# Kernel optimization log

Measured on AMD Instinct MI355X. Metric: run time of the kernel, lower is better.

## Reference

```python
import math
import jax, jax.numpy as jnp
import numpy as np

B, S, DK, DV = 8, 2048, 512, 512

def setup_inputs() -> dict:
    key = jax.random.key(0)
    kq, kk, kv, km = jax.random.split(key, 4)
    Q = jax.random.normal(kq, (B, S, DK), dtype=jnp.float32)
    K = jax.random.normal(kk, (B, S, DK), dtype=jnp.float32)
    V = jax.random.normal(kv, (B, S, DV), dtype=jnp.float32)
    # key-padding mask, True = masked out; broadcasts over query dim
    mask_out = jax.random.randint(km, (B, 1, S), 0, 2).astype(jnp.bool_)
    return {"Q": Q, "K": K, "V": V, "mask_out": mask_out}

def reference(Q, K, V, mask_out):
    scale = math.sqrt(Q.shape[-1])
    # [B, S, S] scores
    scores = jnp.einsum('bqd,bkd->bqk', Q, K) / scale
    scores = jnp.where(mask_out, -jnp.inf, scores)
    attn = jax.nn.softmax(scores, axis=-1)
    # dropout is identity in eval mode (reference baseline)
    return jnp.einsum('bqk,bkv->bqv', attn, V)
```

## Files before the change

kernel.cpp:

```cpp
#include <hip/hip_runtime.h>
#include <stdint.h>
#include <stddef.h>

#define B_ 8
#define S_ 2048
#define D_ 512
#define QT 64
#define KTL 32
#define NIT (S_ / KTL)

typedef __attribute__((ext_vector_type(8))) short short8;
typedef __attribute__((ext_vector_type(4))) float f32x4;

#define OFF_K0  0
#define OFF_K1  32768
#define OFF_ST  65536
#define OFF_P   73728
#define OFF_A   77824
#define OFF_HM  78080
#define OFF_L   78592
#define OFF_M   79104
#define LDS_BYTES 79360

__device__ __forceinline__ void gl_lds16(const void* g, void* l) {
  __builtin_amdgcn_global_load_lds(
      (const __attribute__((address_space(1))) uint32_t*)g,
      (__attribute__((address_space(3))) uint32_t*)l, 16, 0, 0);
}

__device__ __forceinline__ void bar_lgkm() {
  __asm__ __volatile__("" ::: "memory");
  __builtin_amdgcn_s_waitcnt(0xC07F);
  __builtin_amdgcn_s_barrier();
  __asm__ __volatile__("" ::: "memory");
}
__device__ __forceinline__ void bar_vm0() {
  __asm__ __volatile__("" ::: "memory");
  __builtin_amdgcn_s_waitcnt(0x0070);
  __builtin_amdgcn_s_barrier();
  __asm__ __volatile__("" ::: "memory");
}

template<int CTRL>
__device__ __forceinline__ float dpp_mov(float x) {
  return __builtin_bit_cast(float,
      __builtin_amdgcn_update_dpp(0, __builtin_bit_cast(int, x),
                                  CTRL, 0xF, 0xF, true));
}
__device__ __forceinline__ float red8_max(float x) {
  x = fmaxf(x, dpp_mov<0xB1>(x));
  x = fmaxf(x, dpp_mov<0x4E>(x));
  x = fmaxf(x, dpp_mov<0x141>(x));
  return x;
}
__device__ __forceinline__ float red8_sum(float x) {
  x += dpp_mov<0xB1>(x);
  x += dpp_mov<0x4E>(x);
  x += dpp_mov<0x141>(x);
  return x;
}

__device__ __forceinline__ uint32_t f2bf(float f) {
  union { float f; uint32_t u; } x; x.f = f;
  uint32_t r = x.u + 0x7FFFu + ((x.u >> 16) & 1u);
  return r >> 16;
}

__device__ __forceinline__ bool sniff_fp32(const void* p) {
  const uint32_t* w = (const uint32_t*)p;
  bool ok = true;
  #pragma unroll 1
  for (int i = 0; i < 64; ++i) {
    uint32_t e = (w[i] >> 23) & 0xFFu;
    if (!(e == 0u || (e >= 64u && e <= 192u))) ok = false;
  }
  return ok;
}

__device__ __forceinline__ short8 cvt8(const void* src, bool fp32) {
  short8 d;
  if (fp32) {
    const float* s = (const float*)src;
    f32x4 a = *(const f32x4*)s, c = *(const f32x4*)(s + 4);
    #pragma unroll
    for (int j = 0; j < 4; ++j) { d[j] = (short)f2bf(a[j]); d[4 + j] = (short)f2bf(c[j]); }
  } else {
    d = *(const short8*)src;
  }
  return d;
}

__global__ void prep_kernel(const void* __restrict__ K, const void* __restrict__ V,
                            uint16_t* __restrict__ kbf, uint16_t* __restrict__ vt) {
  __shared__ uint32_t vtile[64 * 32];
  bool fp32 = sniff_fp32(K);
  int kt = blockIdx.x, dt = blockIdx.y, b = blockIdx.z;
  int t  = threadIdx.x;
  {
    size_t off = (size_t)b * S_ * D_ + (size_t)(kt * 64 + (t >> 3)) * D_ + dt * 64 + (t & 7) * 8;
    const void* src = fp32 ? (const void*)((const float*)K + off)
                           : (const void*)((const uint16_t*)K + off);
    *(short8*)(kbf + off) = cvt8(src, fp32);
  }
  {
    int key = t >> 3;
    int c0  = (t & 7) * 4;
    size_t off = (size_t)b * S_ * D_ + (size_t)(kt * 64 + key) * D_ + dt * 64 + (t & 7) * 8;
    const void* src = fp32 ? (const void*)((const float*)V + off)
                           : (const void*)((const uint16_t*)V + off);
    short8 d = cvt8(src, fp32);
    const uint32_t* dw = (const uint32_t*)&d;
    #pragma unroll
    for (int i = 0; i < 4; ++i)
      vtile[key * 32 + ((c0 + i + key) & 31)] = dw[i];
  }
  __syncthreads();
  {
    int dvl = t >> 3;
    int kg  = t & 7;
    short8 o;
    #pragma unroll
    for (int j = 0; j < 8; ++j) {
      int key = kg * 8 + j;
      uint32_t wv = vtile[key * 32 + (((dvl >> 1) + key) & 31)];
      o[j] = (short)((dvl & 1) ? (wv >> 16) : (wv & 0xFFFFu));
    }
    *(short8*)(vt + ((size_t)b * D_ + dt * 64 + dvl) * S_ + kt * 64 + kg * 8) = o;
  }
}

__device__ __forceinline__ void stage_K(char* buf, const uint16_t* kg, int w, int lane, int kt) {
  #pragma unroll
  for (int p = 0; p < 4; ++p) {
    int n = p * 8 + w;
    int g = (lane & ~7) | ((lane ^ n) & 7);
    gl_lds16(kg + ((size_t)(kt * KTL + n)) * D_ + g * 8, buf + n * 1024);
  }
}
__device__ __forceinline__ void stage_K_slow(char* buf, const void* kg, bool fp32,
                                             int w, int lane, int kt) {
  #pragma unroll
  for (int p = 0; p < 4; ++p) {
    int n = p * 8 + w;
    size_t off = ((size_t)(kt * KTL + n)) * D_ + lane * 8;
    const void* src = fp32 ? (const void*)((const float*)kg + off)
                           : (const void*)((const uint16_t*)kg + off);
    short8 d = cvt8(src, fp32);
    int s = (lane & ~7) | ((lane ^ n) & 7);
    *(short8*)(buf + n * 1024 + s * 16) = d;
  }
}
__device__ __forceinline__ void stage_V_slow(char* smem, const void* vg, bool fp32,
                                             int w, int lane, int kt) {
  #pragma unroll
  for (int p = 0; p < 4; ++p) {
    int n = p * 8 + w;
    size_t off = ((size_t)(kt * KTL + n)) * D_ + lane * 8;
    const void* src = fp32 ? (const void*)((const float*)vg + off)
                           : (const void*)((const uint16_t*)vg + off);
    short8 d = cvt8(src, fp32);
    *(short8*)(smem + OFF_K1 + n * 1024 + lane * 16) = d;
  }
}

template<bool FAST>
__global__ __launch_bounds__(512, 2)
void attn_kernel(const void* __restrict__ Q, const void* __restrict__ K,
                 const void* __restrict__ V, const void* __restrict__ mask,
                 const uint16_t* __restrict__ kbf, const uint16_t* __restrict__ vtbf,
                 void* __restrict__ out) {
  extern __shared__ char smem[];
  const int tid  = threadIdx.x;
  const int lane = tid & 63;
  const int w    = tid >> 6;
  const int m15  = lane & 15;
  const int kq   = lane >> 4;

  const bool fp32 = sniff_fp32(Q);

  const int b     = blockIdx.x;
  const int qbase = blockIdx.y * QT;
  const int qt_w  = w >> 1;
  const int kh    = w & 1;

  const uint16_t* kgf  = FAST ? (kbf + (size_t)b * S_ * D_) : nullptr;
  const uint16_t* vtg  = FAST ? (vtbf + (size_t)b * D_ * S_) : nullptr;
  const void* kgs = fp32 ? (const void*)((const float*)K + (size_t)b * S_ * D_)
                         : (const void*)((const uint16_t*)K + (size_t)b * S_ * D_);
  const void* vgs = fp32 ? (const void*)((const float*)V + (size_t)b * S_ * D_)
                         : (const void*)((const uint16_t*)V + (size_t)b * S_ * D_);

  if (tid < 64) {
    const uint32_t* mw = (const uint32_t*)mask;
    const uint8_t*  mb = (const uint8_t*)mask;
    bool is64 = true, any_even = false, is32 = true;
    for (int j = 0; j < 64; ++j) {
      uint32_t lo = mw[2 * j], hi = mw[2 * j + 1];
      if (hi != 0u || lo > 1u) is64 = false;
      if (lo) any_even = true;
    }
    is64 = is64 && any_even;
    for (int j = 0; j < 128; ++j) {
      uint32_t x = mw[j];
      if (x != 0u && x != 1u && x != 0x3F800000u) is32 = false;
    }
    uint32_t bits = 0;
    int base = b * S_ + tid * 32;
    for (int e = 0; e < 32; ++e) {
      uint32_t x = is64 ? mw[2 * (base + e)]
                        : (is32 ? mw[base + e] : (uint32_t)mb[base + e]);
      bits |= (x ? 1u : 0u) << e;
    }
    *(uint32_t*)(smem + OFF_M + tid * 4) = bits;
  }

  short8 aq[16];
  {
    size_t q0 = ((size_t)b * S_ + qbase + qt_w * 16 + m15) * D_ + kq * 8;
    #pragma unroll
    for (int sl = 0; sl < 16; ++sl) {
      size_t off = q0 + sl * 32;
      const void* src = fp32 ? (const void*)((const float*)Q + off)
                             : (const void*)((const uint16_t*)Q + off);
      aq[sl] = cvt8(src, fp32);
    }
  }

  f32x4 acc_o[4][4];
  #pragma unroll
  for (int i = 0; i < 4; ++i)
    #pragma unroll
    for (int j = 0; j < 4; ++j)
      acc_o[i][j] = (f32x4){0.f, 0.f, 0.f, 0.f};

  float m_run = -1e30f, l_run = 0.f;
  const float k1 = 0.06375872f;

  const int nql = kh * 16 + m15;
  const int qsw = qt_w * 16 + m15;

  if constexpr (FAST) {
    stage_K(smem + OFF_K0, kgf, w, lane, 0);

    #pragma unroll 1
    for (int kt = 0; kt < NIT; ++kt) {
      char* kbuf = smem + ((kt & 1) ? OFF_K1 : OFF_K0);
      bar_vm0();

      short8 vf[4];
      #pragma unroll
      for (int ct = 0; ct < 4; ++ct)
        vf[ct] = *(const short8*)(vtg + (size_t)(w * 64 + ct * 16 + m15) * S_
                                  + kt * KTL + kq * 8);
      if (kt < NIT - 1)
        stage_K(smem + ((kt & 1) ? OFF_K0 : OFF_K1), kgf, w, lane, kt + 1);

      f32x4 acc_s0 = (f32x4){0.f, 0.f, 0.f, 0.f};
      f32x4 acc_s1 = (f32x4){0.f, 0.f, 0.f, 0.f};
      #pragma unroll
      for (int sl = 0; sl < 8; ++sl) {
        int c0  = sl * 4 + kq;
        int c1  = (sl + 8) * 4 + kq;
        int cs0 = (c0 & ~7) | ((c0 ^ nql) & 7);
        int cs1 = (c1 & ~7) | ((c1 ^ nql) & 7);
        short8 b0 = *(const short8*)(kbuf + nql * 1024 + cs0 * 16);
        short8 b1 = *(const short8*)(kbuf + nql * 1024 + cs1 * 16);
        acc_s0 = __builtin_amdgcn_mfma_f32_16x16x32_bf16(b0, aq[sl],     acc_s0, 0, 0, 0);
        acc_s1 = __builtin_amdgcn_mfma_f32_16x16x32_bf16(b1, aq[sl + 8], acc_s1, 0, 0, 0);
      }

      uint32_t mword = *(const uint32_t*)(smem + OFF_M + kt * 4);
      float u[4];
      #pragma unroll
      for (int r = 0; r < 4; ++r) {
        float bv = ((mword >> (kh * 16 + kq * 4 + r)) & 1u) ? -3.0e38f : 0.f;
        u[r] = (acc_s0[r] + acc_s1[r]) * k1 + bv;
      }
      float hm = fmaxf(fmaxf(u[0], u[1]), fmaxf(u[2], u[3]));
      hm = fmaxf(hm, __shfl_xor(hm, 16, 64));
      hm = fmaxf(hm, __shfl_xor(hm, 32, 64));
      if (lane < 16)
        *(float*)(smem + OFF_HM + qsw * 8 + kh * 4) = hm;
      bar_lgkm();

      float other = *(const float*)(smem + OFF_HM + qsw * 8 + (1 - kh) * 4);
      float m_new = fmaxf(m_run, fmaxf(hm, other));
      float alpha = exp2f(m_run - m_new);
      m_run = m_new;
      float s = 0.f;
      #pragma unroll
      for (int r = 0; r < 4; ++r) { u[r] = exp2f(u[r] - m_new); s += u[r]; }
      s += __shfl_xor(s, 16, 64);
      s += __shfl_xor(s, 32, 64);
      l_run = l_run * alpha + s;
      uint2 d;
      d.x = f2bf(u[0]) | (f2bf(u[1]) << 16);
      d.y = f2bf(u[2]) | (f2bf(u[3]) << 16);
      int g0 = kh * 2 + (kq >> 1);
      int g  = g0 ^ (qsw & 3);
      *(uint2*)(smem + OFF_P + qsw * 64 + g * 16 + (kq & 1) * 8) = d;
      if (kh == 0 && lane < 16)
        *(float*)(smem + OFF_A + qsw * 4) = alpha;
      bar_lgkm();

      #pragma unroll
      for (int rt = 0; rt < 4; ++rt) {
        f32x4 al = *(const f32x4*)(smem + OFF_A + (rt * 16 + kq * 4) * 4);
        #pragma unroll
        for (int ct = 0; ct < 4; ++ct) acc_o[rt][ct] *= al;
      }
      short8 ap[4];
      #pragma unroll
      for (int rt = 0; rt < 4; ++rt) {
        int rr = rt * 16 + m15;
        int gg = kq ^ (rr & 3);
        ap[rt] = *(const short8*)(smem + OFF_P + rr * 64 + gg * 16);
      }
      #pragma unroll
      for (int ct = 0; ct < 4; ++ct)
        #pragma unroll
        for (int rt = 0; rt < 4; ++rt)
          acc_o[rt][ct] = __builtin_amdgcn_mfma_f32_16x16x32_bf16(
              ap[rt], vf[ct], acc_o[rt][ct], 0, 0, 0);
    }

    if (lane < 16)
      *(float*)(smem + OFF_L + qsw * 8 + kh * 4) = l_run;
    __syncthreads();

    #pragma unroll
    for (int rt = 0; rt < 4; ++rt) {
      #pragma unroll
      for (int ct = 0; ct < 4; ++ct) {
        int col = w * 64 + ct * 16 + m15;
        #pragma unroll
        for (int r = 0; r < 4; ++r) {
          int row = rt * 16 + kq * 4 + r;
          float lt = *(const float*)(smem + OFF_L + row * 8)
                   + *(const float*)(smem + OFF_L + row * 8 + 4);
          float inv = lt > 0.f ? 1.f / lt : 0.f;
          size_t idx = ((size_t)b * S_ + qbase + row) * D_ + col;
          float val = acc_o[rt][ct][r] * inv;
          if (fp32) ((float*)out)[idx] = val;
          else      ((uint16_t*)out)[idx] = (uint16_t)f2bf(val);
        }
      }
    }
  } else {
    #pragma unroll 1
    for (int kt = 0; kt < NIT; ++kt) {
      __syncthreads();
      stage_K_slow(smem + OFF_K0, kgs, fp32, w, lane, kt);
      stage_V_slow(smem, vgs, fp32, w, lane, kt);
      __syncthreads();

      int keyg = kt * KTL + nql;
      float bv = ((*(const uint32_t*)(smem + OFF_M + (keyg >> 5) * 4) >> (keyg & 31)) & 1u)
                 ? -3.0e38f : 0.f;
      f32x4 a0 = {0.f,0.f,0.f,0.f}, a1 = {0.f,0.f,0.f,0.f};
      #pragma unroll
      for (int sl = 0; sl < 8; ++sl) {
        int c0  = sl * 4 + kq;
        int c1  = (sl + 8) * 4 + kq;
        int cs0 = (c0 & ~7) | ((c0 ^ nql) & 7);
        int cs1 = (c1 & ~7) | ((c1 ^ nql) & 7);
        short8 bf0 = *(const short8*)(smem + OFF_K0 + nql * 1024 + cs0 * 16);
        short8 bf1 = *(const short8*)(smem + OFF_K0 + nql * 1024 + cs1 * 16);
        a0 = __builtin_amdgcn_mfma_f32_16x16x32_bf16(aq[sl],     bf0, a0, 0, 0, 0);
        a1 = __builtin_amdgcn_mfma_f32_16x16x32_bf16(aq[sl + 8], bf1, a1, 0, 0, 0);
      }
      {
        int blk  = qt_w * 4 + kq;
        int xblk = blk ^ (nql & 15) ^ ((nql >> 2) & 3);
        f32x4 sv;
        #pragma unroll
        for (int r = 0; r < 4; ++r) sv[r] = (a0[r] + a1[r]) * k1 + bv;
        *(f32x4*)(smem + OFF_ST + nql * 256 + xblk * 16) = sv;
      }
      bar_lgkm();

      {
        int r  = w * 8 + (lane >> 3);
        int k0 = (lane & 7) * 4;
        float u[4];
        #pragma unroll
        for (int i = 0; i < 4; ++i) {
          int k    = k0 + i;
          int xblk = (r >> 2) ^ (k & 15) ^ ((k >> 2) & 3);
          u[i] = *(const float*)(smem + OFF_ST + k * 256 + xblk * 16 + (r & 3) * 4);
        }
        float mt = fmaxf(fmaxf(u[0], u[1]), fmaxf(u[2], u[3]));
        mt = red8_max(mt);
        float m_new = fmaxf(m_run, mt);
        float alpha = exp2f(m_run - m_new);
        float s = 0.f;
        #pragma unroll
        for (int i = 0; i < 4; ++i) { u[i] = exp2f(u[i] - m_new); s += u[i]; }
        s = red8_sum(s);
        l_run = l_run * alpha + s;
        m_run = m_new;
        uint2 d;
        d.x = f2bf(u[0]) | (f2bf(u[1]) << 16);
        d.y = f2bf(u[2]) | (f2bf(u[3]) << 16);
        int g = ((lane & 7) >> 1) ^ (r & 3);
        *(uint2*)(smem + OFF_P + r * 64 + g * 16 + (lane & 1) * 8) = d;
        if ((lane & 7) == 0) {
          *(float*)(smem + OFF_A + r * 4) = alpha;
          *(float*)(smem + OFF_L + r * 4) = l_run;
        }
      }
      bar_lgkm();

      #pragma unroll
      for (int rt = 0; rt < 4; ++rt) {
        f32x4 al = *(const f32x4*)(smem + OFF_A + (rt * 16 + kq * 4) * 4);
        #pragma unroll
        for (int ct = 0; ct < 4; ++ct) acc_o[rt][ct] *= al;
      }
      short8 ap[4];
      #pragma unroll
      for (int rt = 0; rt < 4; ++rt) {
        int rr = rt * 16 + m15;
        int g  = kq ^ (rr & 3);
        ap[rt] = *(const short8*)(smem + OFF_P + rr * 64 + g * 16);
      }
      #pragma unroll
      for (int ct = 0; ct < 4; ++ct) {
        short8 bvv;
        #pragma unroll
        for (int j = 0; j < 8; ++j)
          bvv[j] = *(const short*)(smem + OFF_K1 + (kq * 8 + j) * 1024
                                   + (w * 64 + ct * 16 + m15) * 2);
        #pragma unroll
        for (int rt = 0; rt < 4; ++rt)
          acc_o[rt][ct] = __builtin_amdgcn_mfma_f32_16x16x32_bf16(
              ap[rt], bvv, acc_o[rt][ct], 0, 0, 0);
      }
    }

    #pragma unroll
    for (int rt = 0; rt < 4; ++rt) {
      f32x4 lv = *(const f32x4*)(smem + OFF_L + (rt * 16 + kq * 4) * 4);
      f32x4 inv;
      #pragma unroll
      for (int r = 0; r < 4; ++r) inv[r] = lv[r] > 0.f ? 1.f / lv[r] : 0.f;
      #pragma unroll
      for (int ct = 0; ct < 4; ++ct) {
        int col = w * 64 + ct * 16 + m15;
        #pragma unroll
        for (int r = 0; r < 4; ++r) {
          int row = qbase + rt * 16 + kq * 4 + r;
          size_t idx = ((size_t)b * S_ + row) * D_ + col;
          float val = acc_o[rt][ct][r] * inv[r];
          if (fp32) ((float*)out)[idx] = val;
          else      ((uint16_t*)out)[idx] = (uint16_t)f2bf(val);
        }
      }
    }
  }
}

extern "C" void kernel_launch(void* const* d_in, const int* in_sizes, int n_in,
                              void* d_out, int out_size, void* d_ws, size_t ws_size,
                              hipStream_t stream) {
  (void)in_sizes; (void)n_in; (void)out_size;
  const void* Q    = d_in[0];
  const void* K    = d_in[1];
  const void* V    = d_in[2];
  const void* mask = d_in[3];

  const size_t half = (size_t)B_ * S_ * D_ * 2;
  bool fast = ws_size >= 2 * half;

  if (fast) {
    uint16_t* kbf  = (uint16_t*)d_ws;
    uint16_t* vtbf = (uint16_t*)((char*)d_ws + half);
    prep_kernel<<<dim3(32, 8, 8), 512, 0, stream>>>(K, V, kbf, vtbf);
    hipFuncSetAttribute((const void*)attn_kernel<true>,
                        hipFuncAttributeMaxDynamicSharedMemorySize, LDS_BYTES);
    attn_kernel<true><<<dim3(8, S_ / QT), 512, LDS_BYTES, stream>>>(
        Q, K, V, mask, kbf, vtbf, d_out);
  } else {
    hipFuncSetAttribute((const void*)attn_kernel<false>,
                        hipFuncAttributeMaxDynamicSharedMemorySize, LDS_BYTES);
    attn_kernel<false><<<dim3(8, S_ / QT), 512, LDS_BYTES, stream>>>(
        Q, K, V, mask, nullptr, nullptr, d_out);
  }
}
```

Measured before the change: 306.9 us.

## Double key tile to 64 and restructure softmax through staged LDS scores

Raises the per-iteration key tile from 32 to 64 in the fast path, halving the number of barrier-separated iterations. Each wave now computes scores for 32 queries by 16 keys, sharing each K fragment across two MFMAs, and writes them to LDS. A row-wise softmax pass then reads them back with 8-lane reductions instead of cross-wave half-max exchange. LDS use roughly doubles to about 153 KB, which together with 32 Q fragments per thread likely prevents two blocks per CU and adds register pressure.

```diff
diff --git a/kernel.cpp b/kernel.cpp
--- a/kernel.cpp
+++ b/kernel.cpp
@@ -6,21 +6,22 @@
 #define S_ 2048
 #define D_ 512
 #define QT 64
-#define KTL 32
+#define KTL 64
 #define NIT (S_ / KTL)
+#define KTLS 32
+#define NITS (S_ / KTLS)
 
 typedef __attribute__((ext_vector_type(8))) short short8;
 typedef __attribute__((ext_vector_type(4))) float f32x4;
 
 #define OFF_K0  0
-#define OFF_K1  32768
-#define OFF_ST  65536
-#define OFF_P   73728
-#define OFF_A   77824
-#define OFF_HM  78080
-#define OFF_L   78592
-#define OFF_M   79104
-#define LDS_BYTES 79360
+#define OFF_K1  65536
+#define OFF_ST  131072
+#define OFF_P   147456
+#define OFF_A   155648
+#define OFF_L   155904
+#define OFF_M   156160
+#define LDS_BYTES 156416
 
 __device__ __forceinline__ void gl_lds16(const void* g, void* l) {
   __builtin_amdgcn_global_load_lds(
@@ -131,7 +132,7 @@
 
 __device__ __forceinline__ void stage_K(char* buf, const uint16_t* kg, int w, int lane, int kt) {
   #pragma unroll
-  for (int p = 0; p < 4; ++p) {
+  for (int p = 0; p < 8; ++p) {
     int n = p * 8 + w;
     int g = (lane & ~7) | ((lane ^ n) & 7);
     gl_lds16(kg + ((size_t)(kt * KTL + n)) * D_ + g * 8, buf + n * 1024);
@@ -142,7 +143,7 @@
   #pragma unroll
   for (int p = 0; p < 4; ++p) {
     int n = p * 8 + w;
-    size_t off = ((size_t)(kt * KTL + n)) * D_ + lane * 8;
+    size_t off = ((size_t)(kt * KTLS + n)) * D_ + lane * 8;
     const void* src = fp32 ? (const void*)((const float*)kg + off)
                            : (const void*)((const uint16_t*)kg + off);
     short8 d = cvt8(src, fp32);
@@ -155,7 +156,7 @@
   #pragma unroll
   for (int p = 0; p < 4; ++p) {
     int n = p * 8 + w;
-    size_t off = ((size_t)(kt * KTL + n)) * D_ + lane * 8;
+    size_t off = ((size_t)(kt * KTLS + n)) * D_ + lane * 8;
     const void* src = fp32 ? (const void*)((const float*)vg + off)
                            : (const void*)((const uint16_t*)vg + off);
     short8 d = cvt8(src, fp32);
@@ -180,8 +181,6 @@
 
   const int b     = blockIdx.x;
   const int qbase = blockIdx.y * QT;
-  const int qt_w  = w >> 1;
-  const int kh    = w & 1;
 
   const uint16_t* kgf  = FAST ? (kbf + (size_t)b * S_ * D_) : nullptr;
   const uint16_t* vtg  = FAST ? (vtbf + (size_t)b * D_ * S_) : nullptr;
@@ -214,18 +213,6 @@
     *(uint32_t*)(smem + OFF_M + tid * 4) = bits;
   }
 
-  short8 aq[16];
-  {
-    size_t q0 = ((size_t)b * S_ + qbase + qt_w * 16 + m15) * D_ + kq * 8;
-    #pragma unroll
-    for (int sl = 0; sl < 16; ++sl) {
-      size_t off = q0 + sl * 32;
-      const void* src = fp32 ? (const void*)((const float*)Q + off)
-                             : (const void*)((const uint16_t*)Q + off);
-      aq[sl] = cvt8(src, fp32);
-    }
-  }
-
   f32x4 acc_o[4][4];
   #pragma unroll
   for (int i = 0; i < 4; ++i)
@@ -236,10 +223,25 @@
   float m_run = -1e30f, l_run = 0.f;
   const float k1 = 0.06375872f;
 
-  const int nql = kh * 16 + m15;
-  const int qsw = qt_w * 16 + m15;
-
   if constexpr (FAST) {
+    const int qh = w >> 2;
+    const int ks = w & 3;
+    const int n  = ks * 16 + m15;
+
+    short8 aq[32];
+    {
+      size_t q0 = ((size_t)b * S_ + qbase + qh * 32 + m15) * D_ + kq * 8;
+      #pragma unroll
+      for (int sub = 0; sub < 2; ++sub)
+        #pragma unroll
+        for (int sl = 0; sl < 16; ++sl) {
+          size_t off = q0 + (size_t)sub * 16 * D_ + sl * 32;
+          const void* src = fp32 ? (const void*)((const float*)Q + off)
+                                 : (const void*)((const uint16_t*)Q + off);
+          aq[sub * 16 + sl] = cvt8(src, fp32);
+        }
+    }
+
     stage_K(smem + OFF_K0, kgf, w, lane, 0);
 
     #pragma unroll 1
@@ -247,60 +249,80 @@
       char* kbuf = smem + ((kt & 1) ? OFF_K1 : OFF_K0);
       bar_vm0();
 
-      short8 vf[4];
+      short8 vfA[4];
       #pragma unroll
       for (int ct = 0; ct < 4; ++ct)
-        vf[ct] = *(const short8*)(vtg + (size_t)(w * 64 + ct * 16 + m15) * S_
-                                  + kt * KTL + kq * 8);
+        vfA[ct] = *(const short8*)(vtg + (size_t)(w * 64 + ct * 16 + m15) * S_
+                                   + kt * KTL + kq * 8);
       if (kt < NIT - 1)
         stage_K(smem + ((kt & 1) ? OFF_K0 : OFF_K1), kgf, w, lane, kt + 1);
 
-      f32x4 acc_s0 = (f32x4){0.f, 0.f, 0.f, 0.f};
-      f32x4 acc_s1 = (f32x4){0.f, 0.f, 0.f, 0.f};
-      #pragma unroll
-      for (int sl = 0; sl < 8; ++sl) {
-        int c0  = sl * 4 + kq;
-        int c1  = (sl + 8) * 4 + kq;
-        int cs0 = (c0 & ~7) | ((c0 ^ nql) & 7);
-        int cs1 = (c1 & ~7) | ((c1 ^ nql) & 7);
-        short8 b0 = *(const short8*)(kbuf + nql * 1024 + cs0 * 16);
-        short8 b1 = *(const short8*)(kbuf + nql * 1024 + cs1 * 16);
-        acc_s0 = __builtin_amdgcn_mfma_f32_16x16x32_bf16(b0, aq[sl],     acc_s0, 0, 0, 0);
-        acc_s1 = __builtin_amdgcn_mfma_f32_16x16x32_bf16(b1, aq[sl + 8], acc_s1, 0, 0, 0);
-      }
-
-      uint32_t mword = *(const uint32_t*)(smem + OFF_M + kt * 4);
-      float u[4];
-      #pragma unroll
-      for (int r = 0; r < 4; ++r) {
-        float bv = ((mword >> (kh * 16 + kq * 4 + r)) & 1u) ? -3.0e38f : 0.f;
-        u[r] = (acc_s0[r] + acc_s1[r]) * k1 + bv;
-      }
-      float hm = fmaxf(fmaxf(u[0], u[1]), fmaxf(u[2], u[3]));
-      hm = fmaxf(hm, __shfl_xor(hm, 16, 64));
-      hm = fmaxf(hm, __shfl_xor(hm, 32, 64));
-      if (lane < 16)
-        *(float*)(smem + OFF_HM + qsw * 8 + kh * 4) = hm;
+      f32x4 s0 = (f32x4){0.f, 0.f, 0.f, 0.f};
+      f32x4 s1 = (f32x4){0.f, 0.f, 0.f, 0.f};
+      #pragma unroll
+      for (int sl = 0; sl < 16; ++sl) {
+        int c  = sl * 4 + kq;
+        int cs = (c & ~7) | ((c ^ n) & 7);
+        short8 bfr = *(const short8*)(kbuf + n * 1024 + cs * 16);
+        s0 = __builtin_amdgcn_mfma_f32_16x16x32_bf16(aq[sl],      bfr, s0, 0, 0, 0);
+        s1 = __builtin_amdgcn_mfma_f32_16x16x32_bf16(aq[16 + sl], bfr, s1, 0, 0, 0);
+      }
+
+      {
+        int keyg = kt * KTL + n;
+        float bv = ((*(const uint32_t*)(smem + OFF_M + (keyg >> 5) * 4) >> (keyg & 31)) & 1u)
+                   ? -3.0e38f : 0.f;
+        #pragma unroll
+        for (int sub = 0; sub < 2; ++sub) {
+          int blk  = qh * 8 + sub * 4 + kq;
+          int xblk = blk ^ (n & 15) ^ ((n >> 2) & 3) ^ (((n >> 4) & 3) << 1);
+          f32x4 sv;
+          f32x4 sa = sub ? s1 : s0;
+          #pragma unroll
+          for (int r = 0; r < 4; ++r) sv[r] = sa[r] * k1 + bv;
+          *(f32x4*)(smem + OFF_ST + n * 256 + xblk * 16) = sv;
+        }
+      }
+      short8 vfB[4];
+      #pragma unroll
+      for (int ct = 0; ct < 4; ++ct)
+        vfB[ct] = *(const short8*)(vtg + (size_t)(w * 64 + ct * 16 + m15) * S_
+                                   + kt * KTL + 32 + kq * 8);
       bar_lgkm();
 
-      float other = *(const float*)(smem + OFF_HM + qsw * 8 + (1 - kh) * 4);
-      float m_new = fmaxf(m_run, fmaxf(hm, other));
-      float alpha = exp2f(m_run - m_new);
-      m_run = m_new;
-      float s = 0.f;
-      #pragma unroll
-      for (int r = 0; r < 4; ++r) { u[r] = exp2f(u[r] - m_new); s += u[r]; }
-      s += __shfl_xor(s, 16, 64);
-      s += __shfl_xor(s, 32, 64);
-      l_run = l_run * alpha + s;
-      uint2 d;
-      d.x = f2bf(u[0]) | (f2bf(u[1]) << 16);
-      d.y = f2bf(u[2]) | (f2bf(u[3]) << 16);
-      int g0 = kh * 2 + (kq >> 1);
-      int g  = g0 ^ (qsw & 3);
-      *(uint2*)(smem + OFF_P + qsw * 64 + g * 16 + (kq & 1) * 8) = d;
-      if (kh == 0 && lane < 16)
-        *(float*)(smem + OFF_A + qsw * 4) = alpha;
+      {
+        int r  = w * 8 + (lane >> 3);
+        int k0 = (lane & 7) * 8;
+        float u[8];
+        #pragma unroll
+        for (int i = 0; i < 8; ++i) {
+          int k    = k0 + i;
+          int xblk = (r >> 2) ^ (k & 15) ^ ((k >> 2) & 3) ^ (((k >> 4) & 3) << 1);
+          u[i] = *(const float*)(smem + OFF_ST + k * 256 + xblk * 16 + (r & 3) * 4);
+        }
+        float mt = fmaxf(fmaxf(fmaxf(u[0], u[1]), fmaxf(u[2], u[3])),
+                         fmaxf(fmaxf(u[4], u[5]), fmaxf(u[6], u[7])));
+        mt = red8_max(mt);
+        float m_new = fmaxf(m_run, mt);
+        float alpha = exp2f(m_run - m_new);
+        float s = 0.f;
+        #pragma unroll
+        for (int i = 0; i < 8; ++i) { u[i] = exp2f(u[i] - m_new); s += u[i]; }
+        s = red8_sum(s);
+        l_run = l_run * alpha + s;
+        m_run = m_new;
+        uint4 d;
+        d.x = f2bf(u[0]) | (f2bf(u[1]) << 16);
+        d.y = f2bf(u[2]) | (f2bf(u[3]) << 16);
+        d.z = f2bf(u[4]) | (f2bf(u[5]) << 16);
+        d.w = f2bf(u[6]) | (f2bf(u[7]) << 16);
+        int g = (lane & 7) ^ (r & 7);
+        *(uint4*)(smem + OFF_P + r * 128 + g * 16) = d;
+        if ((lane & 7) == 0) {
+          *(float*)(smem + OFF_A + r * 4) = alpha;
+          *(float*)(smem + OFF_L + r * 4) = l_run;
+        }
+      }
       bar_lgkm();
 
       #pragma unroll
@@ -309,52 +331,49 @@
         #pragma unroll
         for (int ct = 0; ct < 4; ++ct) acc_o[rt][ct] *= al;
       }
-      short8 ap[4];
-      #pragma unroll
-      for (int rt = 0; rt < 4; ++rt) {
-        int rr = rt * 16 + m15;
-        int gg = kq ^ (rr & 3);
-        ap[rt] = *(const short8*)(smem + OFF_P + rr * 64 + gg * 16);
-      }
-      #pragma unroll
-      for (int ct = 0; ct < 4; ++ct)
-        #pragma unroll
-        for (int rt = 0; rt < 4; ++rt)
-          acc_o[rt][ct] = __builtin_amdgcn_mfma_f32_16x16x32_bf16(
-              ap[rt], vf[ct], acc_o[rt][ct], 0, 0, 0);
-    }
-
-    if (lane < 16)
-      *(float*)(smem + OFF_L + qsw * 8 + kh * 4) = l_run;
-    __syncthreads();
-
-    #pragma unroll
-    for (int rt = 0; rt < 4; ++rt) {
-      #pragma unroll
-      for (int ct = 0; ct < 4; ++ct) {
-        int col = w * 64 + ct * 16 + m15;
-        #pragma unroll
-        for (int r = 0; r < 4; ++r) {
-          int row = rt * 16 + kq * 4 + r;
-          float lt = *(const float*)(smem + OFF_L + row * 8)
-                   + *(const float*)(smem + OFF_L + row * 8 + 4);
-          float inv = lt > 0.f ? 1.f / lt : 0.f;
-          size_t idx = ((size_t)b * S_ + qbase + row) * D_ + col;
-          float val = acc_o[rt][ct][r] * inv;
-          if (fp32) ((float*)out)[idx] = val;
-          else      ((uint16_t*)out)[idx] = (uint16_t)f2bf(val);
+      #pragma unroll
+      for (int kc = 0; kc < 2; ++kc) {
+        short8 ap[4];
+        #pragma unroll
+        for (int rt = 0; rt < 4; ++rt) {
+          int rr = rt * 16 + m15;
+          int g  = (kc * 4 + kq) ^ (rr & 7);
+          ap[rt] = *(const short8*)(smem + OFF_P + rr * 128 + g * 16);
+        }
+        #pragma unroll
+        for (int ct = 0; ct < 4; ++ct) {
+          short8 bvv = kc ? vfB[ct] : vfA[ct];
+          #pragma unroll
+          for (int rt = 0; rt < 4; ++rt)
+            acc_o[rt][ct] = __builtin_amdgcn_mfma_f32_16x16x32_bf16(
+                ap[rt], bvv, acc_o[rt][ct], 0, 0, 0);
         }
       }
     }
   } else {
+    const int qt_w = w >> 1;
+    const int kh   = w & 1;
+    const int nql  = kh * 16 + m15;
+    short8 aq[16];
+    {
+      size_t q0 = ((size_t)b * S_ + qbase + qt_w * 16 + m15) * D_ + kq * 8;
+      #pragma unroll
+      for (int sl = 0; sl < 16; ++sl) {
+        size_t off = q0 + sl * 32;
+        const void* src = fp32 ? (const void*)((const float*)Q + off)
+                               : (const void*)((const uint16_t*)Q + off);
+        aq[sl] = cvt8(src, fp32);
+      }
+    }
+
     #pragma unroll 1
-    for (int kt = 0; kt < NIT; ++kt) {
+    for (int kt = 0; kt < NITS; ++kt) {
       __syncthreads();
       stage_K_slow(smem + OFF_K0, kgs, fp32, w, lane, kt);
       stage_V_slow(smem, vgs, fp32, w, lane, kt);
       __syncthreads();
 
-      int keyg = kt * KTL + nql;
+      int keyg = kt * KTLS + nql;
       float bv = ((*(const uint32_t*)(smem + OFF_M + (keyg >> 5) * 4) >> (keyg & 31)) & 1u)
                  ? -3.0e38f : 0.f;
       f32x4 a0 = {0.f,0.f,0.f,0.f}, a1 = {0.f,0.f,0.f,0.f};
@@ -437,24 +456,24 @@
               ap[rt], bvv, acc_o[rt][ct], 0, 0, 0);
       }
     }
-
+  }
+
+  #pragma unroll
+  for (int rt = 0; rt < 4; ++rt) {
+    f32x4 lv = *(const f32x4*)(smem + OFF_L + (rt * 16 + kq * 4) * 4);
+    f32x4 inv;
     #pragma unroll
-    for (int rt = 0; rt < 4; ++rt) {
-      f32x4 lv = *(const f32x4*)(smem + OFF_L + (rt * 16 + kq * 4) * 4);
-      f32x4 inv;
-      #pragma unroll
-      for (int r = 0; r < 4; ++r) inv[r] = lv[r] > 0.f ? 1.f / lv[r] : 0.f;
-      #pragma unroll
-      for (int ct = 0; ct < 4; ++ct) {
-        int col = w * 64 + ct * 16 + m15;
-        #pragma unroll
-        for (int r = 0; r < 4; ++r) {
-          int row = qbase + rt * 16 + kq * 4 + r;
-          size_t idx = ((size_t)b * S_ + row) * D_ + col;
-          float val = acc_o[rt][ct][r] * inv[r];
-          if (fp32) ((float*)out)[idx] = val;
-          else      ((uint16_t*)out)[idx] = (uint16_t)f2bf(val);
-        }
+    for (int r = 0; r < 4; ++r) inv[r] = lv[r] > 0.f ? 1.f / lv[r] : 0.f;
+    #pragma unroll
+    for (int ct = 0; ct < 4; ++ct) {
+      int col = w * 64 + ct * 16 + m15;
+      #pragma unroll
+      for (int r = 0; r < 4; ++r) {
+        int row = qbase + rt * 16 + kq * 4 + r;
+        size_t idx = ((size_t)b * S_ + row) * D_ + col;
+        float val = acc_o[rt][ct][r] * inv[r];
+        if (fp32) ((float*)out)[idx] = val;
+        else      ((uint16_t*)out)[idx] = (uint16_t)f2bf(val);
       }
     }
   }
```

Measured after the change: 332.1 us. 8.2% more time.
